# Kernel optimization log

Hardware: AMD Instinct MI355X
Metric: run time of the kernel (lower is better)

The kernel has to match this reference:

```python
import jax, jax.numpy as jnp
import numpy as np

EPS_NORM = 1e-12  # torch F.normalize eps
EPS_PI = 1e-8


def _l2_normalize(x, axis):
    n = jnp.sqrt(jnp.sum(x * x, axis=axis, keepdims=True))
    return x / jnp.maximum(n, EPS_NORM)


def setup_inputs() -> dict:
    key = jax.random.key(0)
    k1, _ = jax.random.split(key)
    B, L, H, E = 8, 1024, 8, 64
    queries = jax.random.normal(k1, (B, L, H, E), dtype=jnp.float32)
    temp = jnp.ones((H, 1), dtype=jnp.float32)  # nn.Parameter(torch.ones(num_heads, 1))
    return {"queries": queries, "temp": temp}


def reference(queries, temp):
    # queries: [B, L, H, E] -> w: [B, H, N, d]
    w = jnp.transpose(queries, (0, 2, 1, 3))
    # normalize over token dim (-2), square, sum over feature dim -> energy [B,H,N]
    w_normed = _l2_normalize(w, axis=-2)
    energy = jnp.sum(w_normed * w_normed, axis=-1)
    # softmax over the HEAD dim (nn.Softmax(dim=1)); temp [H,1] broadcasts over N
    Pi = jax.nn.softmax(energy * temp[None, :, :], axis=1)  # [B,H,N]
    # cosine-similarity attention matrix, mapped to [0,1]
    w_unit = _l2_normalize(w, axis=-1)
    attn_matrix = (jnp.einsum('bhnd,bhmd->bhnm', w_unit, w_unit) + 1.0) * 0.5
    # Pi normalized over tokens
    Pi_norm = Pi / (jnp.sum(Pi, axis=-1, keepdims=True) + EPS_PI)
    # dots: [B,H,1,d] = Pi_norm^T (w**2)
    dots = jnp.einsum('bhn,bhnd->bhd', Pi_norm, w * w)[:, :, None, :]
    attn = 1.0 / (1.0 + dots)  # [B,H,1,d]
    out = -(w * Pi[..., None]) * attn  # [B,H,N,d]
    out = jnp.transpose(out, (0, 2, 1, 3))  # [B,L,H,E]
    attn_reshaped = jnp.transpose(attn_matrix, (0, 2, 1, 3))  # [B,N,H,N]
    return out, attn_reshaped
```

## Files before the change

kernel.cpp:

```cpp
#include <hip/hip_runtime.h>
#include <hip/hip_bf16.h>

#define B_ 8
#define N_ 1024
#define H_ 8
#define D_ 64

typedef __attribute__((ext_vector_type(8))) short short8;
typedef __attribute__((ext_vector_type(4))) float f32x4;

__global__ __launch_bounds__(256) void k_stats(const float* __restrict__ q,
                                               ushort* __restrict__ wunit,
                                               float* __restrict__ energy) {
    const int bh = blockIdx.x;
    const int b = bh >> 3, h = bh & 7;
    const float* qb = q + (size_t)(b * N_ * H_ + h) * D_;
    __shared__ float red[16][64];
    __shared__ float inv2[64];
    const int t = threadIdx.x;
    const int dg = (t & 15) * 4;
    const int ng = t >> 4;

    float ax = 0.f, ay = 0.f, az = 0.f, aw = 0.f;
    for (int n = ng; n < N_; n += 16) {
        const float4 v = *(const float4*)(qb + (size_t)n * (H_ * D_) + dg);
        ax += v.x * v.x; ay += v.y * v.y; az += v.z * v.z; aw += v.w * v.w;
    }
    red[ng][dg + 0] = ax; red[ng][dg + 1] = ay;
    red[ng][dg + 2] = az; red[ng][dg + 3] = aw;
    __syncthreads();
    if (t < 64) {
        float s = 0.f;
        #pragma unroll
        for (int i = 0; i < 16; ++i) s += red[i][t];
        inv2[t] = 1.0f / fmaxf(s, 1e-24f);
    }
    __syncthreads();

    for (int n = t; n < N_; n += 256) {
        const float4* row = (const float4*)(qb + (size_t)n * (H_ * D_));
        float se = 0.f, sr = 0.f;
        #pragma unroll
        for (int i = 0; i < 16; ++i) {
            const float4 v = row[i];
            se += v.x * v.x * inv2[i * 4 + 0] + v.y * v.y * inv2[i * 4 + 1] +
                  v.z * v.z * inv2[i * 4 + 2] + v.w * v.w * inv2[i * 4 + 3];
            sr += v.x * v.x + v.y * v.y + v.z * v.z + v.w * v.w;
        }
        energy[(size_t)bh * N_ + n] = se;
        const float invr = 1.0f / fmaxf(sqrtf(sr), 1e-12f);
        __hip_bfloat162* wrow =
            (__hip_bfloat162*)(wunit + ((size_t)bh * N_ + n) * D_);
        #pragma unroll
        for (int i = 0; i < 16; ++i) {
            const float4 v = row[i];
            wrow[i * 2 + 0] =
                __float22bfloat162_rn(make_float2(v.x * invr, v.y * invr));
            wrow[i * 2 + 1] =
                __float22bfloat162_rn(make_float2(v.z * invr, v.w * invr));
        }
    }
}

__global__ __launch_bounds__(256) void k_pi(const float* __restrict__ energy,
                                            const float* __restrict__ temp,
                                            float* __restrict__ Pi) {
    const int idx = blockIdx.x * 256 + threadIdx.x;
    const int b = idx >> 10, n = idx & (N_ - 1);
    float e[H_];
    float m = -1e30f;
    #pragma unroll
    for (int h = 0; h < H_; ++h) {
        e[h] = energy[((size_t)(b * H_ + h)) * N_ + n] * temp[h];
        m = fmaxf(m, e[h]);
    }
    float s = 0.f;
    #pragma unroll
    for (int h = 0; h < H_; ++h) { e[h] = expf(e[h] - m); s += e[h]; }
    const float inv = 1.0f / s;
    #pragma unroll
    for (int h = 0; h < H_; ++h)
        Pi[((size_t)(b * H_ + h)) * N_ + n] = e[h] * inv;
}

__global__ __launch_bounds__(256) void k_out(const float* __restrict__ q,
                                             const float* __restrict__ Pi,
                                             float* __restrict__ out0) {
    const int bh = blockIdx.x;
    const int b = bh >> 3, h = bh & 7;
    const float* qb = q + (size_t)(b * N_ * H_ + h) * D_;
    const float* Pib = Pi + (size_t)bh * N_;
    __shared__ float red[16][64];
    __shared__ float attnv[64];
    __shared__ float rbuf[256];
    const int t = threadIdx.x;

    float s = 0.f;
    for (int n = t; n < N_; n += 256) s += Pib[n];
    rbuf[t] = s;
    __syncthreads();
    if (t < 64) {
        s = rbuf[t] + rbuf[t + 64] + rbuf[t + 128] + rbuf[t + 192];
        #pragma unroll
        for (int off = 32; off > 0; off >>= 1) s += __shfl_down(s, off);
        if (t == 0) rbuf[0] = 1.0f / (s + 1e-8f);
    }
    __syncthreads();
    const float invS = rbuf[0];

    const int dg = (t & 15) * 4;
    const int ng = t >> 4;
    float ax = 0.f, ay = 0.f, az = 0.f, aw = 0.f;
    for (int n = ng; n < N_; n += 16) {
        const float p = Pib[n];
        const float4 v = *(const float4*)(qb + (size_t)n * (H_ * D_) + dg);
        ax += p * v.x * v.x; ay += p * v.y * v.y;
        az += p * v.z * v.z; aw += p * v.w * v.w;
    }
    red[ng][dg + 0] = ax; red[ng][dg + 1] = ay;
    red[ng][dg + 2] = az; red[ng][dg + 3] = aw;
    __syncthreads();
    if (t < 64) {
        float d2 = 0.f;
        #pragma unroll
        for (int i = 0; i < 16; ++i) d2 += red[i][t];
        attnv[t] = 1.0f / (1.0f + d2 * invS);
    }
    __syncthreads();

    for (int n = t; n < N_; n += 256) {
        const float p = -Pib[n];
        const float4* row = (const float4*)(qb + (size_t)n * (H_ * D_));
        float4* orow = (float4*)(out0 + ((size_t)(b * N_ + n) * H_ + h) * D_);
        #pragma unroll
        for (int i = 0; i < 16; ++i) {
            const float4 v = row[i];
            orow[i] = make_float4(v.x * p * attnv[i * 4 + 0],
                                  v.y * p * attnv[i * 4 + 1],
                                  v.z * p * attnv[i * 4 + 2],
                                  v.w * p * attnv[i * 4 + 3]);
        }
    }
}

__global__ __launch_bounds__(256) void k_gram(const ushort* __restrict__ wunit,
                                              float* __restrict__ out1) {
    const int bh = blockIdx.y;
    const int b = bh >> 3, h = bh & 7;
    const int tn = blockIdx.x & 7;
    const int tm = blockIdx.x >> 3;
    __shared__ ushort lA[128][72];
    __shared__ ushort lB[128][72];
    const int t = threadIdx.x;
    const ushort* Ub = wunit + (size_t)bh * N_ * D_;

    {
        const uint4* gA = (const uint4*)(Ub + (size_t)tn * 128 * D_);
        const uint4* gB = (const uint4*)(Ub + (size_t)tm * 128 * D_);
        #pragma unroll
        for (int c = 0; c < 4; ++c) {
            const int idx = t + c * 256;
            const int row = idx >> 3, col8 = (idx & 7) * 8;
            *(uint4*)&lA[row][col8] = gA[idx];
            *(uint4*)&lB[row][col8] = gB[idx];
        }
    }
    __syncthreads();

    const int wave = t >> 6, lane = t & 63;
    const int rbase = wave * 32;
    const int arow = lane & 15;
    const int kq = (lane >> 4) * 8;

    f32x4 acc[2][8];
    #pragma unroll
    for (int i = 0; i < 2; ++i)
        #pragma unroll
        for (int j = 0; j < 8; ++j) acc[i][j] = (f32x4){0.f, 0.f, 0.f, 0.f};

    #pragma unroll
    for (int kk = 0; kk < 2; ++kk) {
        const int ko = kk * 32 + kq;
        const short8 a0 = *(const short8*)&lA[rbase + arow][ko];
        const short8 a1 = *(const short8*)&lA[rbase + 16 + arow][ko];
        #pragma unroll
        for (int tc = 0; tc < 8; ++tc) {
            const short8 bfr = *(const short8*)&lB[tc * 16 + arow][ko];
            acc[0][tc] = __builtin_amdgcn_mfma_f32_16x16x32_bf16(
                a0, bfr, acc[0][tc], 0, 0, 0);
            acc[1][tc] = __builtin_amdgcn_mfma_f32_16x16x32_bf16(
                a1, bfr, acc[1][tc], 0, 0, 0);
        }
    }

    const int col = lane & 15;
    const int rq = (lane >> 4) * 4;
    #pragma unroll
    for (int tr = 0; tr < 2; ++tr) {
        #pragma unroll
        for (int tc = 0; tc < 8; ++tc) {
            #pragma unroll
            for (int r = 0; r < 4; ++r) {
                const int n = tn * 128 + rbase + tr * 16 + rq + r;
                const int m = tm * 128 + tc * 16 + col;
                out1[((size_t)(b * N_ + n) * H_ + h) * N_ + m] =
                    (acc[tr][tc][r] + 1.0f) * 0.5f;
            }
        }
    }
}

extern "C" void kernel_launch(void* const* d_in, const int* in_sizes, int n_in,
                              void* d_out, int out_size, void* d_ws,
                              size_t ws_size, hipStream_t stream) {
    const float* q = (const float*)d_in[0];
    const float* temp = (const float*)d_in[1];
    float* out0 = (float*)d_out;
    float* out1 = out0 + (size_t)B_ * N_ * H_ * D_;

    ushort* wunit = (ushort*)d_ws;
    float* energy = (float*)((char*)d_ws + (size_t)B_ * H_ * N_ * D_ * 2);
    float* Pi = energy + (size_t)B_ * H_ * N_;

    k_stats<<<B_ * H_, 256, 0, stream>>>(q, wunit, energy);
    k_pi<<<(B_ * N_) / 256, 256, 0, stream>>>(energy, temp, Pi);
    k_out<<<B_ * H_, 256, 0, stream>>>(q, Pi, out0);
    k_gram<<<dim3(64, B_ * H_), 256, 0, stream>>>(wunit, out1);
}
```

Baseline: 385.7 us.

## Split per-head reductions across token chunks with atomics and coalesce Gram stores via LDS

The serial per-(b,h) reductions run on only 64 blocks. They are split into chunked grids (k_colsum, k_energy, k_dots, k_outw) whose partial sums combine through global atomics, with small helper kernels to zero the accumulators and finish the attention weights. The row-wise unit normalisation now uses 16-lane shuffles inside the column-sum pass, and the Pi token sum is accumulated with atomics in k_pi. The Gram kernel stages its MFMA results through shared memory so it can write float4 rows contiguously instead of scattered scalar stores. In exchange there are more kernel launches, atomic float sums with nondeterministic ordering, and an extra pass over q.

```diff
diff --git a/kernel.cpp b/kernel.cpp
--- a/kernel.cpp
+++ b/kernel.cpp
@@ -9,69 +9,86 @@
 typedef __attribute__((ext_vector_type(8))) short short8;
 typedef __attribute__((ext_vector_type(4))) float f32x4;
 
-__global__ __launch_bounds__(256) void k_stats(const float* __restrict__ q,
-                                               ushort* __restrict__ wunit,
-                                               float* __restrict__ energy) {
-    const int bh = blockIdx.x;
+__global__ __launch_bounds__(256) void k_zero(float* __restrict__ p, int n) {
+    const int i = blockIdx.x * 256 + threadIdx.x;
+    if (i < n) p[i] = 0.f;
+}
+
+__global__ __launch_bounds__(256) void k_colsum(const float* __restrict__ q,
+                                                ushort* __restrict__ wunit,
+                                                float* __restrict__ colsum) {
+    const int bh = blockIdx.x, chunk = blockIdx.y;
     const int b = bh >> 3, h = bh & 7;
     const float* qb = q + (size_t)(b * N_ * H_ + h) * D_;
     __shared__ float red[16][64];
-    __shared__ float inv2[64];
-    const int t = threadIdx.x;
-    const int dg = (t & 15) * 4;
+    const int t = threadIdx.x;
     const int ng = t >> 4;
-
-    float ax = 0.f, ay = 0.f, az = 0.f, aw = 0.f;
-    for (int n = ng; n < N_; n += 16) {
-        const float4 v = *(const float4*)(qb + (size_t)n * (H_ * D_) + dg);
-        ax += v.x * v.x; ay += v.y * v.y; az += v.z * v.z; aw += v.w * v.w;
-    }
-    red[ng][dg + 0] = ax; red[ng][dg + 1] = ay;
-    red[ng][dg + 2] = az; red[ng][dg + 3] = aw;
+    const int dq = (t & 15) * 4;
+    float cx = 0.f, cy = 0.f, cz = 0.f, cw = 0.f;
+    #pragma unroll
+    for (int i = 0; i < 8; ++i) {
+        const int n = chunk * 128 + ng + i * 16;
+        const float4 v = *(const float4*)(qb + (size_t)n * (H_ * D_) + dq);
+        cx += v.x * v.x; cy += v.y * v.y; cz += v.z * v.z; cw += v.w * v.w;
+        float ss = v.x * v.x + v.y * v.y + v.z * v.z + v.w * v.w;
+        ss += __shfl_xor(ss, 1, 16);
+        ss += __shfl_xor(ss, 2, 16);
+        ss += __shfl_xor(ss, 4, 16);
+        ss += __shfl_xor(ss, 8, 16);
+        const float invr = 1.0f / fmaxf(sqrtf(ss), 1e-12f);
+        __hip_bfloat162 p0 =
+            __float22bfloat162_rn(make_float2(v.x * invr, v.y * invr));
+        __hip_bfloat162 p1 =
+            __float22bfloat162_rn(make_float2(v.z * invr, v.w * invr));
+        uint2 pk;
+        pk.x = *(unsigned int*)&p0;
+        pk.y = *(unsigned int*)&p1;
+        *(uint2*)(wunit + ((size_t)bh * N_ + n) * D_ + dq) = pk;
+    }
+    red[ng][dq + 0] = cx; red[ng][dq + 1] = cy;
+    red[ng][dq + 2] = cz; red[ng][dq + 3] = cw;
     __syncthreads();
     if (t < 64) {
         float s = 0.f;
         #pragma unroll
         for (int i = 0; i < 16; ++i) s += red[i][t];
-        inv2[t] = 1.0f / fmaxf(s, 1e-24f);
-    }
-    __syncthreads();
-
-    for (int n = t; n < N_; n += 256) {
-        const float4* row = (const float4*)(qb + (size_t)n * (H_ * D_));
-        float se = 0.f, sr = 0.f;
-        #pragma unroll
-        for (int i = 0; i < 16; ++i) {
-            const float4 v = row[i];
-            se += v.x * v.x * inv2[i * 4 + 0] + v.y * v.y * inv2[i * 4 + 1] +
-                  v.z * v.z * inv2[i * 4 + 2] + v.w * v.w * inv2[i * 4 + 3];
-            sr += v.x * v.x + v.y * v.y + v.z * v.z + v.w * v.w;
-        }
-        energy[(size_t)bh * N_ + n] = se;
-        const float invr = 1.0f / fmaxf(sqrtf(sr), 1e-12f);
-        __hip_bfloat162* wrow =
-            (__hip_bfloat162*)(wunit + ((size_t)bh * N_ + n) * D_);
-        #pragma unroll
-        for (int i = 0; i < 16; ++i) {
-            const float4 v = row[i];
-            wrow[i * 2 + 0] =
-                __float22bfloat162_rn(make_float2(v.x * invr, v.y * invr));
-            wrow[i * 2 + 1] =
-                __float22bfloat162_rn(make_float2(v.z * invr, v.w * invr));
-        }
-    }
+        atomicAdd(&colsum[bh * 64 + t], s);
+    }
+}
+
+__global__ __launch_bounds__(256) void k_energy(const float* __restrict__ q,
+                                                const float* __restrict__ colsum,
+                                                float* __restrict__ energy) {
+    const int bh = blockIdx.x, chunk = blockIdx.y;
+    const int b = bh >> 3, h = bh & 7;
+    __shared__ float inv2[64];
+    const int t = threadIdx.x;
+    if (t < 64) inv2[t] = 1.0f / fmaxf(colsum[bh * 64 + t], 1e-24f);
+    __syncthreads();
+    const int n = chunk * 256 + t;
+    const float4* row =
+        (const float4*)(q + (size_t)(b * N_ * H_ + h) * D_ + (size_t)n * (H_ * D_));
+    float e = 0.f;
+    #pragma unroll
+    for (int i = 0; i < 16; ++i) {
+        const float4 v = row[i];
+        e += v.x * v.x * inv2[4 * i + 0] + v.y * v.y * inv2[4 * i + 1] +
+             v.z * v.z * inv2[4 * i + 2] + v.w * v.w * inv2[4 * i + 3];
+    }
+    energy[(size_t)bh * N_ + n] = e;
 }
 
 __global__ __launch_bounds__(256) void k_pi(const float* __restrict__ energy,
                                             const float* __restrict__ temp,
-                                            float* __restrict__ Pi) {
+                                            float* __restrict__ Pi,
+                                            float* __restrict__ Pisum) {
     const int idx = blockIdx.x * 256 + threadIdx.x;
     const int b = idx >> 10, n = idx & (N_ - 1);
     float e[H_];
     float m = -1e30f;
     #pragma unroll
     for (int h = 0; h < H_; ++h) {
-        e[h] = energy[((size_t)(b * H_ + h)) * N_ + n] * temp[h];
+        e[h] = energy[(size_t)(b * H_ + h) * N_ + n] * temp[h];
         m = fmaxf(m, e[h]);
     }
     float s = 0.f;
@@ -79,67 +96,74 @@
     for (int h = 0; h < H_; ++h) { e[h] = expf(e[h] - m); s += e[h]; }
     const float inv = 1.0f / s;
     #pragma unroll
-    for (int h = 0; h < H_; ++h)
-        Pi[((size_t)(b * H_ + h)) * N_ + n] = e[h] * inv;
-}
-
-__global__ __launch_bounds__(256) void k_out(const float* __restrict__ q,
-                                             const float* __restrict__ Pi,
-                                             float* __restrict__ out0) {
-    const int bh = blockIdx.x;
+    for (int h = 0; h < H_; ++h) {
+        const float p = e[h] * inv;
+        Pi[(size_t)(b * H_ + h) * N_ + n] = p;
+        float w = p;
+        #pragma unroll
+        for (int off = 32; off; off >>= 1) w += __shfl_xor(w, off, 64);
+        if ((threadIdx.x & 63) == 0) atomicAdd(&Pisum[b * H_ + h], w);
+    }
+}
+
+__global__ __launch_bounds__(256) void k_dots(const float* __restrict__ q,
+                                              const float* __restrict__ Pi,
+                                              float* __restrict__ dots) {
+    const int bh = blockIdx.x, chunk = blockIdx.y;
     const int b = bh >> 3, h = bh & 7;
     const float* qb = q + (size_t)(b * N_ * H_ + h) * D_;
     const float* Pib = Pi + (size_t)bh * N_;
     __shared__ float red[16][64];
-    __shared__ float attnv[64];
-    __shared__ float rbuf[256];
-    const int t = threadIdx.x;
-
-    float s = 0.f;
-    for (int n = t; n < N_; n += 256) s += Pib[n];
-    rbuf[t] = s;
+    const int t = threadIdx.x, ng = t >> 4, dq = (t & 15) * 4;
+    float cx = 0.f, cy = 0.f, cz = 0.f, cw = 0.f;
+    #pragma unroll
+    for (int i = 0; i < 8; ++i) {
+        const int n = chunk * 128 + ng + i * 16;
+        const float p = Pib[n];
+        const float4 v = *(const float4*)(qb + (size_t)n * (H_ * D_) + dq);
+        cx += p * v.x * v.x; cy += p * v.y * v.y;
+        cz += p * v.z * v.z; cw += p * v.w * v.w;
+    }
+    red[ng][dq + 0] = cx; red[ng][dq + 1] = cy;
+    red[ng][dq + 2] = cz; red[ng][dq + 3] = cw;
     __syncthreads();
     if (t < 64) {
-        s = rbuf[t] + rbuf[t + 64] + rbuf[t + 128] + rbuf[t + 192];
-        #pragma unroll
-        for (int off = 32; off > 0; off >>= 1) s += __shfl_down(s, off);
-        if (t == 0) rbuf[0] = 1.0f / (s + 1e-8f);
-    }
-    __syncthreads();
-    const float invS = rbuf[0];
-
-    const int dg = (t & 15) * 4;
-    const int ng = t >> 4;
-    float ax = 0.f, ay = 0.f, az = 0.f, aw = 0.f;
-    for (int n = ng; n < N_; n += 16) {
-        const float p = Pib[n];
-        const float4 v = *(const float4*)(qb + (size_t)n * (H_ * D_) + dg);
-        ax += p * v.x * v.x; ay += p * v.y * v.y;
-        az += p * v.z * v.z; aw += p * v.w * v.w;
-    }
-    red[ng][dg + 0] = ax; red[ng][dg + 1] = ay;
-    red[ng][dg + 2] = az; red[ng][dg + 3] = aw;
-    __syncthreads();
-    if (t < 64) {
-        float d2 = 0.f;
-        #pragma unroll
-        for (int i = 0; i < 16; ++i) d2 += red[i][t];
-        attnv[t] = 1.0f / (1.0f + d2 * invS);
-    }
-    __syncthreads();
-
-    for (int n = t; n < N_; n += 256) {
-        const float p = -Pib[n];
-        const float4* row = (const float4*)(qb + (size_t)n * (H_ * D_));
-        float4* orow = (float4*)(out0 + ((size_t)(b * N_ + n) * H_ + h) * D_);
-        #pragma unroll
-        for (int i = 0; i < 16; ++i) {
-            const float4 v = row[i];
-            orow[i] = make_float4(v.x * p * attnv[i * 4 + 0],
-                                  v.y * p * attnv[i * 4 + 1],
-                                  v.z * p * attnv[i * 4 + 2],
-                                  v.w * p * attnv[i * 4 + 3]);
-        }
+        float s = 0.f;
+        #pragma unroll
+        for (int i = 0; i < 16; ++i) s += red[i][t];
+        atomicAdd(&dots[bh * 64 + t], s);
+    }
+}
+
+__global__ __launch_bounds__(256) void k_attn(const float* __restrict__ dots,
+                                              const float* __restrict__ Pisum,
+                                              float* __restrict__ attnv) {
+    const int i = blockIdx.x * 256 + threadIdx.x;
+    const int bh = i >> 6;
+    const float invS = 1.0f / (Pisum[bh] + 1e-8f);
+    attnv[i] = 1.0f / (1.0f + dots[i] * invS);
+}
+
+__global__ __launch_bounds__(256) void k_outw(const float* __restrict__ q,
+                                              const float* __restrict__ Pi,
+                                              const float* __restrict__ attnv,
+                                              float* __restrict__ out0) {
+    const int bh = blockIdx.x, chunk = blockIdx.y;
+    const int b = bh >> 3, h = bh & 7;
+    __shared__ float av[64];
+    const int t = threadIdx.x;
+    if (t < 64) av[t] = attnv[bh * 64 + t];
+    __syncthreads();
+    const int n = chunk * 256 + t;
+    const float p = -Pi[(size_t)bh * N_ + n];
+    const float4* row =
+        (const float4*)(q + (size_t)(b * N_ * H_ + h) * D_ + (size_t)n * (H_ * D_));
+    float4* orow = (float4*)(out0 + ((size_t)(b * N_ + n) * H_ + h) * D_);
+    #pragma unroll
+    for (int i = 0; i < 16; ++i) {
+        const float4 v = row[i];
+        orow[i] = make_float4(v.x * p * av[4 * i + 0], v.y * p * av[4 * i + 1],
+                              v.z * p * av[4 * i + 2], v.w * p * av[4 * i + 3]);
     }
 }
 
@@ -147,10 +171,11 @@
                                               float* __restrict__ out1) {
     const int bh = blockIdx.y;
     const int b = bh >> 3, h = bh & 7;
-    const int tn = blockIdx.x & 7;
-    const int tm = blockIdx.x >> 3;
-    __shared__ ushort lA[128][72];
-    __shared__ ushort lB[128][72];
+    const int tn = blockIdx.x & 7, tm = blockIdx.x >> 3;
+    __shared__ __align__(16) char smem[36864];
+    ushort(*lA)[72] = (ushort(*)[72])smem;
+    ushort(*lB)[72] = (ushort(*)[72])(smem + 18432);
+    float* stg = (float*)smem;
     const int t = threadIdx.x;
     const ushort* Ub = wunit + (size_t)bh * N_ * D_;
 
@@ -192,20 +217,26 @@
                 a1, bfr, acc[1][tc], 0, 0, 0);
         }
     }
-
-    const int col = lane & 15;
-    const int rq = (lane >> 4) * 4;
+    __syncthreads();
+
+    float* ms = stg + wave * 2112;
+    const int col = lane & 15, rq = (lane >> 4) * 4;
     #pragma unroll
     for (int tr = 0; tr < 2; ++tr) {
         #pragma unroll
-        for (int tc = 0; tc < 8; ++tc) {
+        for (int tc = 0; tc < 8; ++tc)
             #pragma unroll
-            for (int r = 0; r < 4; ++r) {
-                const int n = tn * 128 + rbase + tr * 16 + rq + r;
-                const int m = tm * 128 + tc * 16 + col;
-                out1[((size_t)(b * N_ + n) * H_ + h) * N_ + m] =
+            for (int r = 0; r < 4; ++r)
+                ms[(rq + r) * 132 + tc * 16 + col] =
                     (acc[tr][tc][r] + 1.0f) * 0.5f;
-            }
+        #pragma unroll
+        for (int i = 0; i < 8; ++i) {
+            const int f = i * 64 + lane;
+            const int r2 = f >> 5, c2 = f & 31;
+            const float4 v = *(const float4*)&ms[r2 * 132 + c2 * 4];
+            const int n = tn * 128 + wave * 32 + tr * 16 + r2;
+            const int m = tm * 128 + c2 * 4;
+            *(float4*)&out1[((size_t)(b * N_ + n) * H_ + h) * N_ + m] = v;
         }
     }
 }
@@ -218,12 +249,21 @@
     float* out0 = (float*)d_out;
     float* out1 = out0 + (size_t)B_ * N_ * H_ * D_;
 
-    ushort* wunit = (ushort*)d_ws;
-    float* energy = (float*)((char*)d_ws + (size_t)B_ * H_ * N_ * D_ * 2);
-    float* Pi = energy + (size_t)B_ * H_ * N_;
-
-    k_stats<<<B_ * H_, 256, 0, stream>>>(q, wunit, energy);
-    k_pi<<<(B_ * N_) / 256, 256, 0, stream>>>(energy, temp, Pi);
-    k_out<<<B_ * H_, 256, 0, stream>>>(q, Pi, out0);
-    k_gram<<<dim3(64, B_ * H_), 256, 0, stream>>>(wunit, out1);
-}
+    char* ws = (char*)d_ws;
+    ushort* wunit = (ushort*)ws;
+    float* Pi     = (float*)(ws + 8388608);
+    float* energy = (float*)(ws + 8650752);
+    float* colsum = (float*)(ws + 8912896);
+    float* dots   = (float*)(ws + 8929280);
+    float* Pisum  = (float*)(ws + 8945664);
+    float* attnv  = (float*)(ws + 8945920);
+
+    k_zero<<<33, 256, 0, stream>>>(colsum, 8256);
+    k_colsum<<<dim3(64, 8), 256, 0, stream>>>(q, wunit, colsum);
+    k_energy<<<dim3(64, 4), 256, 0, stream>>>(q, colsum, energy);
+    k_pi<<<32, 256, 0, stream>>>(energy, temp, Pi, Pisum);
+    k_dots<<<dim3(64, 8), 256, 0, stream>>>(q, Pi, dots);
+    k_attn<<<16, 256, 0, stream>>>(dots, Pisum, attnv);
+    k_outw<<<dim3(64, 4), 256, 0, stream>>>(q, Pi, attnv, out0);
+    k_gram<<<dim3(64, 64), 256, 0, stream>>>(wunit, out1);
+}
```

New measurement: 335.7 us. 1.15x faster.
